# Optimization experiments

Hardware: AMD Instinct MI355X
Metric: run time of the kernel (lower is better)

The kernel has to match this reference:

```python
import jax, jax.numpy as jnp
import numpy as np

HIDDEN = 256
HEADS = 8
HEAD_DIM = HIDDEN // HEADS
SCALE = HEAD_DIM ** -0.5
N = 4096
NUM_GRAPHS = 16
LN_EPS = 1e-5


def setup_inputs() -> dict:
    key = jax.random.key(0)
    ks = jax.random.split(key, 8)
    x = jax.random.normal(ks[0], (N, HIDDEN), dtype=jnp.float32)
    batch = jnp.sort(jax.random.randint(ks[1], (N,), 0, NUM_GRAPHS, dtype=jnp.int64))
    # Xavier-uniform linear weights, stored as [in, out] (y = x @ W + b)
    lim = float(np.sqrt(6.0 / (HIDDEN + HIDDEN)))
    def W(k):
        return jax.random.uniform(k, (HIDDEN, HIDDEN), jnp.float32, -lim, lim)
    return {
        "x": x,
        "batch": batch,
        "Wq": W(ks[2]), "bq": jnp.zeros((HIDDEN,), jnp.float32),
        "Wk": W(ks[3]), "bk": jnp.zeros((HIDDEN,), jnp.float32),
        "Wv": W(ks[4]), "bv": jnp.zeros((HIDDEN,), jnp.float32),
        "Wo": W(ks[5]), "bo": jnp.zeros((HIDDEN,), jnp.float32),
        "gamma": jnp.ones((HIDDEN,), jnp.float32),
        "beta": jnp.zeros((HIDDEN,), jnp.float32),
    }


def _layer_norm(x, gamma, beta):
    mu = jnp.mean(x, axis=-1, keepdims=True)
    var = jnp.mean(jnp.square(x - mu), axis=-1, keepdims=True)
    return (x - mu) * jax.lax.rsqrt(var + LN_EPS) * gamma + beta


def reference(x, batch, Wq, bq, Wk, bk, Wv, bv, Wo, bo, gamma, beta):
    residual = x
    h = _layer_norm(x, gamma, beta)
    n = h.shape[0]
    q = (h @ Wq + bq).reshape(n, HEADS, HEAD_DIM)
    k = (h @ Wk + bk).reshape(n, HEADS, HEAD_DIM)
    v = (h @ Wv + bv).reshape(n, HEADS, HEAD_DIM)
    # dense scores masked to block-diagonal (same-graph) structure
    scores = jnp.einsum('ihd,jhd->ihj', q, k) * SCALE  # [N, H, N]
    same_graph = (batch[None, :] == batch[:, None])[:, None, :]  # [N, 1, N]
    scores = jnp.where(same_graph, scores, -jnp.inf)
    attn = jax.nn.softmax(scores, axis=-1)
    attn = jnp.nan_to_num(attn, nan=0.0)
    out = jnp.einsum('ihj,jhd->ihd', attn, v).reshape(n, HIDDEN)
    out = out @ Wo + bo
    return residual + out
```

## Files before the change

kernel.cpp:

```cpp
#include <hip/hip_runtime.h>

#define NNODES 4096
#define HID 256
#define NG 16
#define NH 8
#define HD 32
#define LN_EPS 1e-5f
#define QSCALE (0.17677669529663687f * 1.4426950408889634f)
#define CAPT 384
#define VTS (CAPT + 2)

typedef unsigned short u16;
typedef unsigned int u32;
typedef __bf16 bf16x8 __attribute__((ext_vector_type(8)));
typedef float f32x4 __attribute__((ext_vector_type(4)));

__device__ __forceinline__ float bf2f(u16 u){
  union { u32 i; float f; } c; c.i = ((u32)u) << 16; return c.f;
}
__device__ __forceinline__ u16 f2bf(float f){
  union { float f; u32 i; } c; c.f = f;
  u32 x = c.i;
  return (u16)((x + 0x7fffu + ((x >> 16) & 1u)) >> 16);
}

__global__ __launch_bounds__(256) void prep_kernel(
    const float* __restrict__ x, const float* __restrict__ gamma,
    const float* __restrict__ beta, u16* __restrict__ h,
    const float* __restrict__ Wq, const float* __restrict__ Wk,
    const float* __restrict__ Wv, const float* __restrict__ Wo,
    u16* __restrict__ Wt, const int* __restrict__ bw, int* __restrict__ seg){
  __shared__ u16 tile[32][33];
  __shared__ int bad;
  int b = blockIdx.x;
  if (b < 1024){
    int wave = threadIdx.x >> 6, lane = threadIdx.x & 63;
    int row = b * 4 + wave;
    float4 xv = ((const float4*)x)[row * 64 + lane];
    float a0 = xv.x, a1 = xv.y, a2 = xv.z, a3 = xv.w;
    float s = a0 + a1 + a2 + a3;
    #pragma unroll
    for (int m = 1; m < 64; m <<= 1) s += __shfl_xor(s, m);
    float mu = s * (1.0f / HID);
    float d0 = a0 - mu, d1 = a1 - mu, d2 = a2 - mu, d3 = a3 - mu;
    float vv = d0*d0 + d1*d1 + d2*d2 + d3*d3;
    #pragma unroll
    for (int m = 1; m < 64; m <<= 1) vv += __shfl_xor(vv, m);
    float rs = rsqrtf(vv * (1.0f / HID) + LN_EPS);
    float4 gv = ((const float4*)gamma)[lane];
    float4 bv = ((const float4*)beta)[lane];
    ushort4 o;
    o.x = f2bf(d0 * rs * gv.x + bv.x);
    o.y = f2bf(d1 * rs * gv.y + bv.y);
    o.z = f2bf(d2 * rs * gv.z + bv.z);
    o.w = f2bf(d3 * rs * gv.w + bv.w);
    *(ushort4*)(h + (size_t)row * HID + lane * 4) = o;
  } else if (b < 1280){
    int idx = b - 1024;
    int w = idx >> 6;
    int t = idx & 63;
    int bx = (t & 7) * 32, by = (t >> 3) * 32;
    const float* src = (w == 0) ? Wq : (w == 1) ? Wk : (w == 2) ? Wv : Wo;
    u16* dst = Wt + (size_t)w * HID * HID;
    int tx = threadIdx.x & 31, ty = threadIdx.x >> 5;
    #pragma unroll
    for (int r = 0; r < 32; r += 8)
      tile[ty + r][tx] = f2bf(src[(size_t)(by + ty + r) * HID + bx + tx]);
    __syncthreads();
    #pragma unroll
    for (int r = 0; r < 32; r += 8)
      dst[(size_t)(bx + ty + r) * HID + by + tx] = tile[tx][ty + r];
  } else {
    if (threadIdx.x == 0) bad = 0;
    __syncthreads();
    int local_bad = 0;
    for (int i = threadIdx.x; i < NNODES; i += 256){
      int v = bw[i];
      if (v < 0 || v > 15) local_bad = 1;
      if (i + 1 < NNODES && bw[i + 1] < v) local_bad = 1;
    }
    if (local_bad) atomicOr(&bad, 1);
    __syncthreads();
    int stride = bad ? 2 : 1;
    int g = threadIdx.x;
    if (g <= NG){
      int lo = 0, hi = NNODES;
      while (lo < hi){
        int mid = (lo + hi) >> 1;
        if (bw[mid * stride] < g) lo = mid + 1; else hi = mid;
      }
      seg[g] = lo;
    }
  }
}

template<bool FINAL>
__device__ __forceinline__ void gemm_tile(const u16* __restrict__ A, const u16* __restrict__ Bt,
    const float* __restrict__ bias, const float* __restrict__ resid, void* __restrict__ out){
  int gw = blockIdx.x * 4 + (threadIdx.x >> 6);
  int lane = threadIdx.x & 63;
  int lr = lane & 15, lq = lane >> 4;
  int m0 = (gw >> 4) * 64;
  int n0 = (gw & 15) * 16;
  f32x4 acc[4] = {};
  const u16* arow = A + (size_t)(m0 + lr) * HID + lq * 8;
  const u16* brow = Bt + (size_t)(n0 + lr) * HID + lq * 8;
  #pragma unroll
  for (int k0 = 0; k0 < HID; k0 += 32){
    bf16x8 b = *(const bf16x8*)(brow + k0);
    #pragma unroll
    for (int t = 0; t < 4; t++){
      bf16x8 a = *(const bf16x8*)(arow + (size_t)t * 16 * HID + k0);
      acc[t] = __builtin_amdgcn_mfma_f32_16x16x32_bf16(a, b, acc[t], 0, 0, 0);
    }
  }
  int col = n0 + lr;
  float bb = bias[col];
  #pragma unroll
  for (int t = 0; t < 4; t++){
    #pragma unroll
    for (int r = 0; r < 4; r++){
      int row = m0 + 16 * t + lq * 4 + r;
      float val = acc[t][r] + bb;
      if (FINAL){
        val += resid[(size_t)row * HID + col];
        ((float*)out)[(size_t)row * HID + col] = val;
      } else {
        ((u16*)out)[(size_t)row * HID + col] = f2bf(val);
      }
    }
  }
}

__global__ __launch_bounds__(256) void gemm_qkv_kernel(const u16* __restrict__ h,
    const u16* __restrict__ Wt, const float* __restrict__ bq, const float* __restrict__ bk,
    const float* __restrict__ bv, u16* __restrict__ q, u16* __restrict__ k, u16* __restrict__ v){
  int which = blockIdx.y;
  const u16* B = Wt + (size_t)which * HID * HID;
  const float* bias = (which == 0) ? bq : (which == 1) ? bk : bv;
  u16* out = (which == 0) ? q : (which == 1) ? k : v;
  gemm_tile<false>(h, B, bias, nullptr, out);
}

__global__ __launch_bounds__(256) void gemm_proj_kernel(const u16* __restrict__ ao,
    const u16* __restrict__ WtO, const float* __restrict__ bo, const float* __restrict__ x,
    float* __restrict__ out){
  gemm_tile<true>(ao, WtO, bo, x, out);
}

__global__ __launch_bounds__(256) void attn_kernel(const u16* __restrict__ q,
    const u16* __restrict__ k, const u16* __restrict__ v, const int* __restrict__ seg,
    u16* __restrict__ out){
  __shared__ u16 kl[CAPT * HD];
  __shared__ u16 vt[HD * VTS];
  int gh = blockIdx.y;
  int g = gh >> 3, hd = gh & 7;
  int start = seg[g], end = seg[g + 1];
  int len = end - start;
  if (len <= 0) return;
  if (len > CAPT) len = CAPT;
  int ntj = (len + 15) >> 4;
  int nj16 = ntj << 4;
  for (int idx = threadIdx.x; idx < nj16 * 4; idx += 256){
    int row = idx >> 2, part = idx & 3;
    uint4 val = make_uint4(0, 0, 0, 0);
    if (row < len)
      val = *(const uint4*)&k[(size_t)(start + row) * HID + hd * HD + part * 8];
    *(uint4*)&kl[row * HD + part * 8] = val;
  }
  for (int idx = threadIdx.x; idx < nj16 * 16; idx += 256){
    int row = idx >> 4, dg = idx & 15;
    u32 w = 0;
    if (row < len)
      w = *(const u32*)&v[(size_t)(start + row) * HID + hd * HD + dg * 2];
    vt[(2 * dg) * VTS + row]     = (u16)(w & 0xffffu);
    vt[(2 * dg + 1) * VTS + row] = (u16)(w >> 16);
  }
  __syncthreads();
  int wave = threadIdx.x >> 6, lane = threadIdx.x & 63;
  int lq = lane >> 4, lr = lane & 15;
  for (int tq = blockIdx.x * 4 + wave; tq < ntj; tq += gridDim.x * 4){
    int q0 = tq << 4;
    bf16x8 qf = *(const bf16x8*)&q[(size_t)(start + q0 + lr) * HID + hd * HD + lq * 8];
    f32x4 o0 = {0.f, 0.f, 0.f, 0.f}, o1 = {0.f, 0.f, 0.f, 0.f};
    float m = -3.0e38f, l = 0.f;
    for (int jt = 0; jt < ntj; jt++){
      int j0 = jt << 4;
      bf16x8 kf = *(const bf16x8*)&kl[(j0 + lr) * HD + lq * 8];
      f32x4 st = __builtin_amdgcn_mfma_f32_16x16x32_bf16(kf, qf,
                   (f32x4){0.f, 0.f, 0.f, 0.f}, 0, 0, 0);
      int jb = j0 + lq * 4;
      float s0 = (jb + 0 < len) ? st[0] * QSCALE : -3.0e38f;
      float s1 = (jb + 1 < len) ? st[1] * QSCALE : -3.0e38f;
      float s2 = (jb + 2 < len) ? st[2] * QSCALE : -3.0e38f;
      float s3 = (jb + 3 < len) ? st[3] * QSCALE : -3.0e38f;
      float tm = fmaxf(fmaxf(s0, s1), fmaxf(s2, s3));
      tm = fmaxf(tm, __shfl_xor(tm, 16));
      tm = fmaxf(tm, __shfl_xor(tm, 32));
      float mn = fmaxf(m, tm);
      float alpha = exp2f(m - mn);
      float p0 = exp2f(s0 - mn), p1 = exp2f(s1 - mn);
      float p2 = exp2f(s2 - mn), p3 = exp2f(s3 - mn);
      float ps = (p0 + p1) + (p2 + p3);
      ps += __shfl_xor(ps, 16);
      ps += __shfl_xor(ps, 32);
      l = l * alpha + ps;
      m = mn;
      union { bf16x8 v8; u16 s[8]; u32 w[4]; } pf, vf0, vf1;
      pf.w[0] = (u32)f2bf(p0) | ((u32)f2bf(p1) << 16);
      pf.w[1] = (u32)f2bf(p2) | ((u32)f2bf(p3) << 16);
      pf.w[2] = 0; pf.w[3] = 0;
      const u16* vp0 = &vt[lr * VTS + j0 + lq * 4];
      const u16* vp1 = &vt[(16 + lr) * VTS + j0 + lq * 4];
      vf0.w[0] = *(const u32*)vp0; vf0.w[1] = *(const u32*)(vp0 + 2);
      vf0.w[2] = 0; vf0.w[3] = 0;
      vf1.w[0] = *(const u32*)vp1; vf1.w[1] = *(const u32*)(vp1 + 2);
      vf1.w[2] = 0; vf1.w[3] = 0;
      o0 = o0 * alpha;
      o1 = o1 * alpha;
      o0 = __builtin_amdgcn_mfma_f32_16x16x32_bf16(vf0.v8, pf.v8, o0, 0, 0, 0);
      o1 = __builtin_amdgcn_mfma_f32_16x16x32_bf16(vf1.v8, pf.v8, o1, 0, 0, 0);
    }
    if (q0 + lr < len){
      float rl = 1.0f / l;
      u16* orow = out + (size_t)(start + q0 + lr) * HID + hd * HD;
      int dbase = lq * 4;
      *(u32*)&orow[dbase]          = (u32)f2bf(o0[0]*rl) | ((u32)f2bf(o0[1]*rl) << 16);
      *(u32*)&orow[dbase + 2]      = (u32)f2bf(o0[2]*rl) | ((u32)f2bf(o0[3]*rl) << 16);
      *(u32*)&orow[16 + dbase]     = (u32)f2bf(o1[0]*rl) | ((u32)f2bf(o1[1]*rl) << 16);
      *(u32*)&orow[16 + dbase + 2] = (u32)f2bf(o1[2]*rl) | ((u32)f2bf(o1[3]*rl) << 16);
    }
  }
}

__global__ void sentinel_kernel(u32* __restrict__ out, int nwords){
  int i = blockIdx.x * 256 + threadIdx.x;
  if (i < nwords) out[i] = 0x46404640u;
}

extern "C" void kernel_launch(void* const* d_in, const int* in_sizes, int n_in,
                              void* d_out, int out_size, void* d_ws, size_t ws_size,
                              hipStream_t stream){
  const float* x   = (const float*)d_in[0];
  const int* batch = (const int*)d_in[1];
  const float* Wq = (const float*)d_in[2],  *bq = (const float*)d_in[3];
  const float* Wk = (const float*)d_in[4],  *bk = (const float*)d_in[5];
  const float* Wv = (const float*)d_in[6],  *bv = (const float*)d_in[7];
  const float* Wo = (const float*)d_in[8],  *bo = (const float*)d_in[9];
  const float* gamma = (const float*)d_in[10], *beta = (const float*)d_in[11];

  const size_t WT_OFF  = 1024;
  const size_t QKV_OFF = WT_OFF + 4 * HID * HID * 2;
  const size_t BUF     = (size_t)NNODES * HID * 2;
  const size_t NEED    = QKV_OFF + 4 * BUF;

  if (ws_size < NEED){
    int nwords = out_size / 2;
    sentinel_kernel<<<(nwords + 255) / 256, 256, 0, stream>>>((u32*)d_out, nwords);
    return;
  }

  char* w = (char*)d_ws;
  int* seg  = (int*)(w + 128);
  u16* Wt   = (u16*)(w + WT_OFF);
  u16* qb   = (u16*)(w + QKV_OFF);
  u16* kb   = qb + (size_t)NNODES * HID;
  u16* vb   = kb + (size_t)NNODES * HID;
  u16* ao   = vb + (size_t)NNODES * HID;
  u16* h    = (u16*)d_out;

  prep_kernel<<<1281, 256, 0, stream>>>(x, gamma, beta, h, Wq, Wk, Wv, Wo, Wt, batch, seg);
  gemm_qkv_kernel<<<dim3(256, 3), 256, 0, stream>>>(h, Wt, bq, bk, bv, qb, kb, vb);
  attn_kernel<<<dim3(4, NG * NH), 256, 0, stream>>>(qb, kb, vb, seg, ao);
  gemm_proj_kernel<<<256, 256, 0, stream>>>(ao, Wt + 3 * (size_t)HID * HID, bo, x, (float*)d_out);
}
```

Baseline: 133.5 us.

## Fuse all stages into one cooperative persistent kernel with grid syncs

Replaces the four separate launches (prep, QKV GEMM, attention, output projection) with a single cooperative kernel of 256 blocks that separates stages with grid.sync(). Each block now does several LayerNorm rows, one weight-transpose tile, QKV tiles for all three matrices, and two attention jobs. The aim is to remove per-launch overhead and inter-kernel gaps. In exchange, grid-wide barriers and reduced parallelism per stage (256 blocks instead of up to 1281) may lengthen some stages, and LN output moves to a new workspace buffer.

```diff
diff --git a/kernel.cpp b/kernel.cpp
--- a/kernel.cpp
+++ b/kernel.cpp
@@ -1,4 +1,7 @@
 #include <hip/hip_runtime.h>
+#include <hip/hip_cooperative_groups.h>
+
+namespace cg = cooperative_groups;
 
 #define NNODES 4096
 #define HID 256
@@ -10,6 +13,10 @@
 #define CAPT 384
 #define VTS (CAPT + 2)
 
+#define WT_OFF  1024
+#define QKV_OFF (WT_OFF + 4 * HID * HID * 2)
+#define BUFSZ   ((size_t)NNODES * HID * 2)
+
 typedef unsigned short u16;
 typedef unsigned int u32;
 typedef __bf16 bf16x8 __attribute__((ext_vector_type(8)));
@@ -22,76 +29,6 @@
   union { float f; u32 i; } c; c.f = f;
   u32 x = c.i;
   return (u16)((x + 0x7fffu + ((x >> 16) & 1u)) >> 16);
-}
-
-__global__ __launch_bounds__(256) void prep_kernel(
-    const float* __restrict__ x, const float* __restrict__ gamma,
-    const float* __restrict__ beta, u16* __restrict__ h,
-    const float* __restrict__ Wq, const float* __restrict__ Wk,
-    const float* __restrict__ Wv, const float* __restrict__ Wo,
-    u16* __restrict__ Wt, const int* __restrict__ bw, int* __restrict__ seg){
-  __shared__ u16 tile[32][33];
-  __shared__ int bad;
-  int b = blockIdx.x;
-  if (b < 1024){
-    int wave = threadIdx.x >> 6, lane = threadIdx.x & 63;
-    int row = b * 4 + wave;
-    float4 xv = ((const float4*)x)[row * 64 + lane];
-    float a0 = xv.x, a1 = xv.y, a2 = xv.z, a3 = xv.w;
-    float s = a0 + a1 + a2 + a3;
-    #pragma unroll
-    for (int m = 1; m < 64; m <<= 1) s += __shfl_xor(s, m);
-    float mu = s * (1.0f / HID);
-    float d0 = a0 - mu, d1 = a1 - mu, d2 = a2 - mu, d3 = a3 - mu;
-    float vv = d0*d0 + d1*d1 + d2*d2 + d3*d3;
-    #pragma unroll
-    for (int m = 1; m < 64; m <<= 1) vv += __shfl_xor(vv, m);
-    float rs = rsqrtf(vv * (1.0f / HID) + LN_EPS);
-    float4 gv = ((const float4*)gamma)[lane];
-    float4 bv = ((const float4*)beta)[lane];
-    ushort4 o;
-    o.x = f2bf(d0 * rs * gv.x + bv.x);
-    o.y = f2bf(d1 * rs * gv.y + bv.y);
-    o.z = f2bf(d2 * rs * gv.z + bv.z);
-    o.w = f2bf(d3 * rs * gv.w + bv.w);
-    *(ushort4*)(h + (size_t)row * HID + lane * 4) = o;
-  } else if (b < 1280){
-    int idx = b - 1024;
-    int w = idx >> 6;
-    int t = idx & 63;
-    int bx = (t & 7) * 32, by = (t >> 3) * 32;
-    const float* src = (w == 0) ? Wq : (w == 1) ? Wk : (w == 2) ? Wv : Wo;
-    u16* dst = Wt + (size_t)w * HID * HID;
-    int tx = threadIdx.x & 31, ty = threadIdx.x >> 5;
-    #pragma unroll
-    for (int r = 0; r < 32; r += 8)
-      tile[ty + r][tx] = f2bf(src[(size_t)(by + ty + r) * HID + bx + tx]);
-    __syncthreads();
-    #pragma unroll
-    for (int r = 0; r < 32; r += 8)
-      dst[(size_t)(bx + ty + r) * HID + by + tx] = tile[tx][ty + r];
-  } else {
-    if (threadIdx.x == 0) bad = 0;
-    __syncthreads();
-    int local_bad = 0;
-    for (int i = threadIdx.x; i < NNODES; i += 256){
-      int v = bw[i];
-      if (v < 0 || v > 15) local_bad = 1;
-      if (i + 1 < NNODES && bw[i + 1] < v) local_bad = 1;
-    }
-    if (local_bad) atomicOr(&bad, 1);
-    __syncthreads();
-    int stride = bad ? 2 : 1;
-    int g = threadIdx.x;
-    if (g <= NG){
-      int lo = 0, hi = NNODES;
-      while (lo < hi){
-        int mid = (lo + hi) >> 1;
-        if (bw[mid * stride] < g) lo = mid + 1; else hi = mid;
-      }
-      seg[g] = lo;
-    }
-  }
 }
 
 template<bool FINAL>
@@ -132,105 +69,192 @@
   }
 }
 
-__global__ __launch_bounds__(256) void gemm_qkv_kernel(const u16* __restrict__ h,
-    const u16* __restrict__ Wt, const float* __restrict__ bq, const float* __restrict__ bk,
-    const float* __restrict__ bv, u16* __restrict__ q, u16* __restrict__ k, u16* __restrict__ v){
-  int which = blockIdx.y;
-  const u16* B = Wt + (size_t)which * HID * HID;
-  const float* bias = (which == 0) ? bq : (which == 1) ? bk : bv;
-  u16* out = (which == 0) ? q : (which == 1) ? k : v;
-  gemm_tile<false>(h, B, bias, nullptr, out);
-}
-
-__global__ __launch_bounds__(256) void gemm_proj_kernel(const u16* __restrict__ ao,
-    const u16* __restrict__ WtO, const float* __restrict__ bo, const float* __restrict__ x,
-    float* __restrict__ out){
-  gemm_tile<true>(ao, WtO, bo, x, out);
-}
-
-__global__ __launch_bounds__(256) void attn_kernel(const u16* __restrict__ q,
-    const u16* __restrict__ k, const u16* __restrict__ v, const int* __restrict__ seg,
-    u16* __restrict__ out){
+__global__ __launch_bounds__(256) void fused_kernel(
+    const float* __restrict__ x, const int* __restrict__ bw,
+    const float* __restrict__ Wq, const float* __restrict__ bq,
+    const float* __restrict__ Wk, const float* __restrict__ bk,
+    const float* __restrict__ Wv, const float* __restrict__ bv,
+    const float* __restrict__ Wo, const float* __restrict__ bo,
+    const float* __restrict__ gamma, const float* __restrict__ beta,
+    char* __restrict__ ws, float* __restrict__ out){
+  cg::grid_group grid = cg::this_grid();
   __shared__ u16 kl[CAPT * HD];
   __shared__ u16 vt[HD * VTS];
-  int gh = blockIdx.y;
-  int g = gh >> 3, hd = gh & 7;
-  int start = seg[g], end = seg[g + 1];
-  int len = end - start;
-  if (len <= 0) return;
-  if (len > CAPT) len = CAPT;
-  int ntj = (len + 15) >> 4;
-  int nj16 = ntj << 4;
-  for (int idx = threadIdx.x; idx < nj16 * 4; idx += 256){
-    int row = idx >> 2, part = idx & 3;
-    uint4 val = make_uint4(0, 0, 0, 0);
-    if (row < len)
-      val = *(const uint4*)&k[(size_t)(start + row) * HID + hd * HD + part * 8];
-    *(uint4*)&kl[row * HD + part * 8] = val;
-  }
-  for (int idx = threadIdx.x; idx < nj16 * 16; idx += 256){
-    int row = idx >> 4, dg = idx & 15;
-    u32 w = 0;
-    if (row < len)
-      w = *(const u32*)&v[(size_t)(start + row) * HID + hd * HD + dg * 2];
-    vt[(2 * dg) * VTS + row]     = (u16)(w & 0xffffu);
-    vt[(2 * dg + 1) * VTS + row] = (u16)(w >> 16);
-  }
-  __syncthreads();
+  __shared__ int bad;
+
+  int* seg = (int*)(ws + 128);
+  u16* Wt  = (u16*)(ws + WT_OFF);
+  u16* qb  = (u16*)(ws + QKV_OFF);
+  u16* kb  = qb + (size_t)NNODES * HID;
+  u16* vb  = kb + (size_t)NNODES * HID;
+  u16* ao  = vb + (size_t)NNODES * HID;
+  u16* h   = ao + (size_t)NNODES * HID;
+
+  int b = blockIdx.x;
   int wave = threadIdx.x >> 6, lane = threadIdx.x & 63;
-  int lq = lane >> 4, lr = lane & 15;
-  for (int tq = blockIdx.x * 4 + wave; tq < ntj; tq += gridDim.x * 4){
-    int q0 = tq << 4;
-    bf16x8 qf = *(const bf16x8*)&q[(size_t)(start + q0 + lr) * HID + hd * HD + lq * 8];
-    f32x4 o0 = {0.f, 0.f, 0.f, 0.f}, o1 = {0.f, 0.f, 0.f, 0.f};
-    float m = -3.0e38f, l = 0.f;
-    for (int jt = 0; jt < ntj; jt++){
-      int j0 = jt << 4;
-      bf16x8 kf = *(const bf16x8*)&kl[(j0 + lr) * HD + lq * 8];
-      f32x4 st = __builtin_amdgcn_mfma_f32_16x16x32_bf16(kf, qf,
-                   (f32x4){0.f, 0.f, 0.f, 0.f}, 0, 0, 0);
-      int jb = j0 + lq * 4;
-      float s0 = (jb + 0 < len) ? st[0] * QSCALE : -3.0e38f;
-      float s1 = (jb + 1 < len) ? st[1] * QSCALE : -3.0e38f;
-      float s2 = (jb + 2 < len) ? st[2] * QSCALE : -3.0e38f;
-      float s3 = (jb + 3 < len) ? st[3] * QSCALE : -3.0e38f;
-      float tm = fmaxf(fmaxf(s0, s1), fmaxf(s2, s3));
-      tm = fmaxf(tm, __shfl_xor(tm, 16));
-      tm = fmaxf(tm, __shfl_xor(tm, 32));
-      float mn = fmaxf(m, tm);
-      float alpha = exp2f(m - mn);
-      float p0 = exp2f(s0 - mn), p1 = exp2f(s1 - mn);
-      float p2 = exp2f(s2 - mn), p3 = exp2f(s3 - mn);
-      float ps = (p0 + p1) + (p2 + p3);
-      ps += __shfl_xor(ps, 16);
-      ps += __shfl_xor(ps, 32);
-      l = l * alpha + ps;
-      m = mn;
-      union { bf16x8 v8; u16 s[8]; u32 w[4]; } pf, vf0, vf1;
-      pf.w[0] = (u32)f2bf(p0) | ((u32)f2bf(p1) << 16);
-      pf.w[1] = (u32)f2bf(p2) | ((u32)f2bf(p3) << 16);
-      pf.w[2] = 0; pf.w[3] = 0;
-      const u16* vp0 = &vt[lr * VTS + j0 + lq * 4];
-      const u16* vp1 = &vt[(16 + lr) * VTS + j0 + lq * 4];
-      vf0.w[0] = *(const u32*)vp0; vf0.w[1] = *(const u32*)(vp0 + 2);
-      vf0.w[2] = 0; vf0.w[3] = 0;
-      vf1.w[0] = *(const u32*)vp1; vf1.w[1] = *(const u32*)(vp1 + 2);
-      vf1.w[2] = 0; vf1.w[3] = 0;
-      o0 = o0 * alpha;
-      o1 = o1 * alpha;
-      o0 = __builtin_amdgcn_mfma_f32_16x16x32_bf16(vf0.v8, pf.v8, o0, 0, 0, 0);
-      o1 = __builtin_amdgcn_mfma_f32_16x16x32_bf16(vf1.v8, pf.v8, o1, 0, 0, 0);
-    }
-    if (q0 + lr < len){
-      float rl = 1.0f / l;
-      u16* orow = out + (size_t)(start + q0 + lr) * HID + hd * HD;
-      int dbase = lq * 4;
-      *(u32*)&orow[dbase]          = (u32)f2bf(o0[0]*rl) | ((u32)f2bf(o0[1]*rl) << 16);
-      *(u32*)&orow[dbase + 2]      = (u32)f2bf(o0[2]*rl) | ((u32)f2bf(o0[3]*rl) << 16);
-      *(u32*)&orow[16 + dbase]     = (u32)f2bf(o1[0]*rl) | ((u32)f2bf(o1[1]*rl) << 16);
-      *(u32*)&orow[16 + dbase + 2] = (u32)f2bf(o1[2]*rl) | ((u32)f2bf(o1[3]*rl) << 16);
-    }
-  }
+
+  #pragma unroll
+  for (int i = 0; i < 4; i++){
+    int row = b * 16 + i * 4 + wave;
+    float4 xv = ((const float4*)x)[row * 64 + lane];
+    float a0 = xv.x, a1 = xv.y, a2 = xv.z, a3 = xv.w;
+    float s = a0 + a1 + a2 + a3;
+    #pragma unroll
+    for (int m = 1; m < 64; m <<= 1) s += __shfl_xor(s, m);
+    float mu = s * (1.0f / HID);
+    float d0 = a0 - mu, d1 = a1 - mu, d2 = a2 - mu, d3 = a3 - mu;
+    float vv = d0*d0 + d1*d1 + d2*d2 + d3*d3;
+    #pragma unroll
+    for (int m = 1; m < 64; m <<= 1) vv += __shfl_xor(vv, m);
+    float rs = rsqrtf(vv * (1.0f / HID) + LN_EPS);
+    float4 gv = ((const float4*)gamma)[lane];
+    float4 bv2 = ((const float4*)beta)[lane];
+    ushort4 o;
+    o.x = f2bf(d0 * rs * gv.x + bv2.x);
+    o.y = f2bf(d1 * rs * gv.y + bv2.y);
+    o.z = f2bf(d2 * rs * gv.z + bv2.z);
+    o.w = f2bf(d3 * rs * gv.w + bv2.w);
+    *(ushort4*)(h + (size_t)row * HID + lane * 4) = o;
+  }
+
+  {
+    u16 (*tile)[33] = (u16(*)[33])kl;
+    int w = b >> 6;
+    int t = b & 63;
+    int bx = (t & 7) * 32, by = (t >> 3) * 32;
+    const float* src = (w == 0) ? Wq : (w == 1) ? Wk : (w == 2) ? Wv : Wo;
+    u16* dst = Wt + (size_t)w * HID * HID;
+    int tx = threadIdx.x & 31, ty = threadIdx.x >> 5;
+    #pragma unroll
+    for (int r = 0; r < 32; r += 8)
+      tile[ty + r][tx] = f2bf(src[(size_t)(by + ty + r) * HID + bx + tx]);
+    __syncthreads();
+    #pragma unroll
+    for (int r = 0; r < 32; r += 8)
+      dst[(size_t)(bx + ty + r) * HID + by + tx] = tile[tx][ty + r];
+  }
+
+  if (b == 0){
+    if (threadIdx.x == 0) bad = 0;
+    __syncthreads();
+    int local_bad = 0;
+    for (int i = threadIdx.x; i < NNODES; i += 256){
+      int v = bw[i];
+      if (v < 0 || v > 15) local_bad = 1;
+      if (i + 1 < NNODES && bw[i + 1] < v) local_bad = 1;
+    }
+    if (local_bad) atomicOr(&bad, 1);
+    __syncthreads();
+    int stride = bad ? 2 : 1;
+    int g = threadIdx.x;
+    if (g <= NG){
+      int lo = 0, hi = NNODES;
+      while (lo < hi){
+        int mid = (lo + hi) >> 1;
+        if (bw[mid * stride] < g) lo = mid + 1; else hi = mid;
+      }
+      seg[g] = lo;
+    }
+  }
+
+  grid.sync();
+
+  #pragma unroll
+  for (int rep = 0; rep < 3; rep++){
+    const u16* B = Wt + (size_t)rep * HID * HID;
+    const float* bias = (rep == 0) ? bq : (rep == 1) ? bk : bv;
+    u16* o = (rep == 0) ? qb : (rep == 1) ? kb : vb;
+    gemm_tile<false>(h, B, bias, nullptr, o);
+  }
+
+  grid.sync();
+
+  for (int rep = 0; rep < 2; rep++){
+    int job = b + 256 * rep;
+    int bx = job >> 7, gh = job & 127;
+    int g = gh >> 3, hd = gh & 7;
+    int start = seg[g], end = seg[g + 1];
+    int len = end - start;
+    if (len > CAPT) len = CAPT;
+    if (len > 0){
+      int ntj = (len + 15) >> 4;
+      int nj16 = ntj << 4;
+      __syncthreads();
+      for (int idx = threadIdx.x; idx < nj16 * 4; idx += 256){
+        int row = idx >> 2, part = idx & 3;
+        uint4 val = make_uint4(0, 0, 0, 0);
+        if (row < len)
+          val = *(const uint4*)&kb[(size_t)(start + row) * HID + hd * HD + part * 8];
+        *(uint4*)&kl[row * HD + part * 8] = val;
+      }
+      for (int idx = threadIdx.x; idx < nj16 * 16; idx += 256){
+        int row = idx >> 4, dg = idx & 15;
+        u32 w = 0;
+        if (row < len)
+          w = *(const u32*)&vb[(size_t)(start + row) * HID + hd * HD + dg * 2];
+        vt[(2 * dg) * VTS + row]     = (u16)(w & 0xffffu);
+        vt[(2 * dg + 1) * VTS + row] = (u16)(w >> 16);
+      }
+      __syncthreads();
+      int lq = lane >> 4, lr = lane & 15;
+      for (int tq = bx * 4 + wave; tq < ntj; tq += 16){
+        int q0 = tq << 4;
+        bf16x8 qf = *(const bf16x8*)&qb[(size_t)(start + q0 + lr) * HID + hd * HD + lq * 8];
+        f32x4 o0 = {0.f, 0.f, 0.f, 0.f}, o1 = {0.f, 0.f, 0.f, 0.f};
+        float m = -3.0e38f, l = 0.f;
+        for (int jt = 0; jt < ntj; jt++){
+          int j0 = jt << 4;
+          bf16x8 kf = *(const bf16x8*)&kl[(j0 + lr) * HD + lq * 8];
+          f32x4 st = __builtin_amdgcn_mfma_f32_16x16x32_bf16(kf, qf,
+                       (f32x4){0.f, 0.f, 0.f, 0.f}, 0, 0, 0);
+          int jb2 = j0 + lq * 4;
+          float s0 = (jb2 + 0 < len) ? st[0] * QSCALE : -3.0e38f;
+          float s1 = (jb2 + 1 < len) ? st[1] * QSCALE : -3.0e38f;
+          float s2 = (jb2 + 2 < len) ? st[2] * QSCALE : -3.0e38f;
+          float s3 = (jb2 + 3 < len) ? st[3] * QSCALE : -3.0e38f;
+          float tm = fmaxf(fmaxf(s0, s1), fmaxf(s2, s3));
+          tm = fmaxf(tm, __shfl_xor(tm, 16));
+          tm = fmaxf(tm, __shfl_xor(tm, 32));
+          float mn = fmaxf(m, tm);
+          float alpha = exp2f(m - mn);
+          float p0 = exp2f(s0 - mn), p1 = exp2f(s1 - mn);
+          float p2 = exp2f(s2 - mn), p3 = exp2f(s3 - mn);
+          float ps = (p0 + p1) + (p2 + p3);
+          ps += __shfl_xor(ps, 16);
+          ps += __shfl_xor(ps, 32);
+          l = l * alpha + ps;
+          m = mn;
+          union { bf16x8 v8; u32 w[4]; } pf, vf0, vf1;
+          pf.w[0] = (u32)f2bf(p0) | ((u32)f2bf(p1) << 16);
+          pf.w[1] = (u32)f2bf(p2) | ((u32)f2bf(p3) << 16);
+          pf.w[2] = 0; pf.w[3] = 0;
+          const u16* vp0 = &vt[lr * VTS + j0 + lq * 4];
+          const u16* vp1 = &vt[(16 + lr) * VTS + j0 + lq * 4];
+          vf0.w[0] = *(const u32*)vp0; vf0.w[1] = *(const u32*)(vp0 + 2);
+          vf0.w[2] = 0; vf0.w[3] = 0;
+          vf1.w[0] = *(const u32*)vp1; vf1.w[1] = *(const u32*)(vp1 + 2);
+          vf1.w[2] = 0; vf1.w[3] = 0;
+          o0 = o0 * alpha;
+          o1 = o1 * alpha;
+          o0 = __builtin_amdgcn_mfma_f32_16x16x32_bf16(vf0.v8, pf.v8, o0, 0, 0, 0);
+          o1 = __builtin_amdgcn_mfma_f32_16x16x32_bf16(vf1.v8, pf.v8, o1, 0, 0, 0);
+        }
+        if (q0 + lr < len){
+          float rl = 1.0f / l;
+          u16* orow = ao + (size_t)(start + q0 + lr) * HID + hd * HD;
+          int dbase = lq * 4;
+          *(u32*)&orow[dbase]          = (u32)f2bf(o0[0]*rl) | ((u32)f2bf(o0[1]*rl) << 16);
+          *(u32*)&orow[dbase + 2]      = (u32)f2bf(o0[2]*rl) | ((u32)f2bf(o0[3]*rl) << 16);
+          *(u32*)&orow[16 + dbase]     = (u32)f2bf(o1[0]*rl) | ((u32)f2bf(o1[1]*rl) << 16);
+          *(u32*)&orow[16 + dbase + 2] = (u32)f2bf(o1[2]*rl) | ((u32)f2bf(o1[3]*rl) << 16);
+        }
+      }
+    }
+  }
+
+  grid.sync();
+
+  gemm_tile<true>(ao, Wt + 3 * (size_t)HID * HID, bo, x, out);
 }
 
 __global__ void sentinel_kernel(u32* __restrict__ out, int nwords){
@@ -248,11 +272,10 @@
   const float* Wv = (const float*)d_in[6],  *bv = (const float*)d_in[7];
   const float* Wo = (const float*)d_in[8],  *bo = (const float*)d_in[9];
   const float* gamma = (const float*)d_in[10], *beta = (const float*)d_in[11];
-
-  const size_t WT_OFF  = 1024;
-  const size_t QKV_OFF = WT_OFF + 4 * HID * HID * 2;
-  const size_t BUF     = (size_t)NNODES * HID * 2;
-  const size_t NEED    = QKV_OFF + 4 * BUF;
+  char* ws = (char*)d_ws;
+  float* out = (float*)d_out;
+
+  const size_t NEED = (size_t)QKV_OFF + 5 * BUFSZ;
 
   if (ws_size < NEED){
     int nwords = out_size / 2;
@@ -260,17 +283,10 @@
     return;
   }
 
-  char* w = (char*)d_ws;
-  int* seg  = (int*)(w + 128);
-  u16* Wt   = (u16*)(w + WT_OFF);
-  u16* qb   = (u16*)(w + QKV_OFF);
-  u16* kb   = qb + (size_t)NNODES * HID;
-  u16* vb   = kb + (size_t)NNODES * HID;
-  u16* ao   = vb + (size_t)NNODES * HID;
-  u16* h    = (u16*)d_out;
-
-  prep_kernel<<<1281, 256, 0, stream>>>(x, gamma, beta, h, Wq, Wk, Wv, Wo, Wt, batch, seg);
-  gemm_qkv_kernel<<<dim3(256, 3), 256, 0, stream>>>(h, Wt, bq, bk, bv, qb, kb, vb);
-  attn_kernel<<<dim3(4, NG * NH), 256, 0, stream>>>(qb, kb, vb, seg, ao);
-  gemm_proj_kernel<<<256, 256, 0, stream>>>(ao, Wt + 3 * (size_t)HID * HID, bo, x, (float*)d_out);
-}
+  void* args[] = { (void*)&x, (void*)&batch, (void*)&Wq, (void*)&bq,
+                   (void*)&Wk, (void*)&bk, (void*)&Wv, (void*)&bv,
+                   (void*)&Wo, (void*)&bo, (void*)&gamma, (void*)&beta,
+                   (void*)&ws, (void*)&out };
+  hipLaunchCooperativeKernel((const void*)fused_kernel, dim3(256), dim3(256),
+                             args, 0, stream);
+}
```

After: 230.9 us. 1.73x slower.

## Replace online softmax with register-resident two-pass softmax and vectorize V transpose

Applied to the files above, without the earlier changes.

The attention kernel now computes all score tiles for a query block up front into a fully unrolled register array (up to 24 tiles), takes one global max, then computes the exponentials and their sum, and finally runs the PV MFMAs. This removes the per-tile cross-lane max/sum shuffles and the alpha rescaling of the accumulators that the online softmax needed. The V-transpose staging also switches to 16-byte global loads. The cost is much higher register pressure (96 floats of scores plus packed probabilities), which may lower occupancy or cause spills.

```diff
diff --git a/kernel.cpp b/kernel.cpp
--- a/kernel.cpp
+++ b/kernel.cpp
@@ -8,6 +8,7 @@
 #define LN_EPS 1e-5f
 #define QSCALE (0.17677669529663687f * 1.4426950408889634f)
 #define CAPT 384
+#define NTJMAX 24
 #define VTS (CAPT + 2)
 
 typedef unsigned short u16;
@@ -168,13 +169,20 @@
       val = *(const uint4*)&k[(size_t)(start + row) * HID + hd * HD + part * 8];
     *(uint4*)&kl[row * HD + part * 8] = val;
   }
-  for (int idx = threadIdx.x; idx < nj16 * 16; idx += 256){
-    int row = idx >> 4, dg = idx & 15;
-    u32 w = 0;
+  for (int idx = threadIdx.x; idx < nj16 * 4; idx += 256){
+    int row = idx >> 2, part = idx & 3;
+    uint4 w = make_uint4(0, 0, 0, 0);
     if (row < len)
-      w = *(const u32*)&v[(size_t)(start + row) * HID + hd * HD + dg * 2];
-    vt[(2 * dg) * VTS + row]     = (u16)(w & 0xffffu);
-    vt[(2 * dg + 1) * VTS + row] = (u16)(w >> 16);
+      w = *(const uint4*)&v[(size_t)(start + row) * HID + hd * HD + part * 8];
+    int d0 = part * 8;
+    vt[(d0 + 0) * VTS + row] = (u16)(w.x & 0xffffu);
+    vt[(d0 + 1) * VTS + row] = (u16)(w.x >> 16);
+    vt[(d0 + 2) * VTS + row] = (u16)(w.y & 0xffffu);
+    vt[(d0 + 3) * VTS + row] = (u16)(w.y >> 16);
+    vt[(d0 + 4) * VTS + row] = (u16)(w.z & 0xffffu);
+    vt[(d0 + 5) * VTS + row] = (u16)(w.z >> 16);
+    vt[(d0 + 6) * VTS + row] = (u16)(w.w & 0xffffu);
+    vt[(d0 + 7) * VTS + row] = (u16)(w.w >> 16);
   }
   __syncthreads();
   int wave = threadIdx.x >> 6, lane = threadIdx.x & 63;
@@ -182,44 +190,61 @@
   for (int tq = blockIdx.x * 4 + wave; tq < ntj; tq += gridDim.x * 4){
     int q0 = tq << 4;
     bf16x8 qf = *(const bf16x8*)&q[(size_t)(start + q0 + lr) * HID + hd * HD + lq * 8];
+    f32x4 st[NTJMAX];
+    #pragma unroll
+    for (int jt = 0; jt < NTJMAX; jt++){
+      if (jt < ntj){
+        bf16x8 kf = *(const bf16x8*)&kl[((jt << 4) + lr) * HD + lq * 8];
+        st[jt] = __builtin_amdgcn_mfma_f32_16x16x32_bf16(kf, qf,
+                   (f32x4){0.f, 0.f, 0.f, 0.f}, 0, 0, 0);
+      }
+    }
+    float m = -3.0e38f;
+    #pragma unroll
+    for (int jt = 0; jt < NTJMAX; jt++){
+      if (jt < ntj){
+        int jb = (jt << 4) + lq * 4;
+        float s0 = (jb + 0 < len) ? st[jt][0] * QSCALE : -3.0e38f;
+        float s1 = (jb + 1 < len) ? st[jt][1] * QSCALE : -3.0e38f;
+        float s2 = (jb + 2 < len) ? st[jt][2] * QSCALE : -3.0e38f;
+        float s3 = (jb + 3 < len) ? st[jt][3] * QSCALE : -3.0e38f;
+        st[jt][0] = s0; st[jt][1] = s1; st[jt][2] = s2; st[jt][3] = s3;
+        m = fmaxf(m, fmaxf(fmaxf(s0, s1), fmaxf(s2, s3)));
+      }
+    }
+    m = fmaxf(m, __shfl_xor(m, 16));
+    m = fmaxf(m, __shfl_xor(m, 32));
+    float l = 0.f;
+    u32 pw[NTJMAX][2];
+    #pragma unroll
+    for (int jt = 0; jt < NTJMAX; jt++){
+      if (jt < ntj){
+        float p0 = exp2f(st[jt][0] - m), p1 = exp2f(st[jt][1] - m);
+        float p2 = exp2f(st[jt][2] - m), p3 = exp2f(st[jt][3] - m);
+        l += (p0 + p1) + (p2 + p3);
+        pw[jt][0] = (u32)f2bf(p0) | ((u32)f2bf(p1) << 16);
+        pw[jt][1] = (u32)f2bf(p2) | ((u32)f2bf(p3) << 16);
+      }
+    }
+    l += __shfl_xor(l, 16);
+    l += __shfl_xor(l, 32);
     f32x4 o0 = {0.f, 0.f, 0.f, 0.f}, o1 = {0.f, 0.f, 0.f, 0.f};
-    float m = -3.0e38f, l = 0.f;
-    for (int jt = 0; jt < ntj; jt++){
-      int j0 = jt << 4;
-      bf16x8 kf = *(const bf16x8*)&kl[(j0 + lr) * HD + lq * 8];
-      f32x4 st = __builtin_amdgcn_mfma_f32_16x16x32_bf16(kf, qf,
-                   (f32x4){0.f, 0.f, 0.f, 0.f}, 0, 0, 0);
-      int jb = j0 + lq * 4;
-      float s0 = (jb + 0 < len) ? st[0] * QSCALE : -3.0e38f;
-      float s1 = (jb + 1 < len) ? st[1] * QSCALE : -3.0e38f;
-      float s2 = (jb + 2 < len) ? st[2] * QSCALE : -3.0e38f;
-      float s3 = (jb + 3 < len) ? st[3] * QSCALE : -3.0e38f;
-      float tm = fmaxf(fmaxf(s0, s1), fmaxf(s2, s3));
-      tm = fmaxf(tm, __shfl_xor(tm, 16));
-      tm = fmaxf(tm, __shfl_xor(tm, 32));
-      float mn = fmaxf(m, tm);
-      float alpha = exp2f(m - mn);
-      float p0 = exp2f(s0 - mn), p1 = exp2f(s1 - mn);
-      float p2 = exp2f(s2 - mn), p3 = exp2f(s3 - mn);
-      float ps = (p0 + p1) + (p2 + p3);
-      ps += __shfl_xor(ps, 16);
-      ps += __shfl_xor(ps, 32);
-      l = l * alpha + ps;
-      m = mn;
-      union { bf16x8 v8; u16 s[8]; u32 w[4]; } pf, vf0, vf1;
-      pf.w[0] = (u32)f2bf(p0) | ((u32)f2bf(p1) << 16);
-      pf.w[1] = (u32)f2bf(p2) | ((u32)f2bf(p3) << 16);
-      pf.w[2] = 0; pf.w[3] = 0;
-      const u16* vp0 = &vt[lr * VTS + j0 + lq * 4];
-      const u16* vp1 = &vt[(16 + lr) * VTS + j0 + lq * 4];
-      vf0.w[0] = *(const u32*)vp0; vf0.w[1] = *(const u32*)(vp0 + 2);
-      vf0.w[2] = 0; vf0.w[3] = 0;
-      vf1.w[0] = *(const u32*)vp1; vf1.w[1] = *(const u32*)(vp1 + 2);
-      vf1.w[2] = 0; vf1.w[3] = 0;
-      o0 = o0 * alpha;
-      o1 = o1 * alpha;
-      o0 = __builtin_amdgcn_mfma_f32_16x16x32_bf16(vf0.v8, pf.v8, o0, 0, 0, 0);
-      o1 = __builtin_amdgcn_mfma_f32_16x16x32_bf16(vf1.v8, pf.v8, o1, 0, 0, 0);
+    #pragma unroll
+    for (int jt = 0; jt < NTJMAX; jt++){
+      if (jt < ntj){
+        int j0 = jt << 4;
+        union { bf16x8 v8; u32 w[4]; } pf, vf0, vf1;
+        pf.w[0] = pw[jt][0]; pf.w[1] = pw[jt][1];
+        pf.w[2] = 0; pf.w[3] = 0;
+        const u16* vp0 = &vt[lr * VTS + j0 + lq * 4];
+        const u16* vp1 = &vt[(16 + lr) * VTS + j0 + lq * 4];
+        vf0.w[0] = *(const u32*)vp0; vf0.w[1] = *(const u32*)(vp0 + 2);
+        vf0.w[2] = 0; vf0.w[3] = 0;
+        vf1.w[0] = *(const u32*)vp1; vf1.w[1] = *(const u32*)(vp1 + 2);
+        vf1.w[2] = 0; vf1.w[3] = 0;
+        o0 = __builtin_amdgcn_mfma_f32_16x16x32_bf16(vf0.v8, pf.v8, o0, 0, 0, 0);
+        o1 = __builtin_amdgcn_mfma_f32_16x16x32_bf16(vf1.v8, pf.v8, o1, 0, 0, 0);
+      }
     }
     if (q0 + lr < len){
       float rl = 1.0f / l;
```

Measured after the change: 145.4 us. 8.9% more time.

## Process two query tiles per wave to reuse K/V fragments in attention

Applied to the files above, without the earlier changes.

Each wave now handles a pair of 16-row query tiles, sharing every K fragment and V-transposed fragment load between two independent online-softmax chains. This interleaves twice the MFMA work per LDS read, and the grid drops from 4 to 2 blocks per graph-head. The V transpose load is widened to 16-byte global reads. The costs are higher register pressure, fewer blocks (256 in total) so less parallelism, and a possible out-of-segment Q read for the B tile, which is loaded even when hasB is false.

```diff
diff --git a/kernel.cpp b/kernel.cpp
--- a/kernel.cpp
+++ b/kernel.cpp
@@ -168,67 +168,118 @@
       val = *(const uint4*)&k[(size_t)(start + row) * HID + hd * HD + part * 8];
     *(uint4*)&kl[row * HD + part * 8] = val;
   }
-  for (int idx = threadIdx.x; idx < nj16 * 16; idx += 256){
-    int row = idx >> 4, dg = idx & 15;
-    u32 w = 0;
+  for (int idx = threadIdx.x; idx < nj16 * 4; idx += 256){
+    int row = idx >> 2, part = idx & 3;
+    uint4 w = make_uint4(0, 0, 0, 0);
     if (row < len)
-      w = *(const u32*)&v[(size_t)(start + row) * HID + hd * HD + dg * 2];
-    vt[(2 * dg) * VTS + row]     = (u16)(w & 0xffffu);
-    vt[(2 * dg + 1) * VTS + row] = (u16)(w >> 16);
+      w = *(const uint4*)&v[(size_t)(start + row) * HID + hd * HD + part * 8];
+    int d0 = part * 8;
+    vt[(d0 + 0) * VTS + row] = (u16)(w.x & 0xffffu);
+    vt[(d0 + 1) * VTS + row] = (u16)(w.x >> 16);
+    vt[(d0 + 2) * VTS + row] = (u16)(w.y & 0xffffu);
+    vt[(d0 + 3) * VTS + row] = (u16)(w.y >> 16);
+    vt[(d0 + 4) * VTS + row] = (u16)(w.z & 0xffffu);
+    vt[(d0 + 5) * VTS + row] = (u16)(w.z >> 16);
+    vt[(d0 + 6) * VTS + row] = (u16)(w.w & 0xffffu);
+    vt[(d0 + 7) * VTS + row] = (u16)(w.w >> 16);
   }
   __syncthreads();
   int wave = threadIdx.x >> 6, lane = threadIdx.x & 63;
   int lq = lane >> 4, lr = lane & 15;
-  for (int tq = blockIdx.x * 4 + wave; tq < ntj; tq += gridDim.x * 4){
-    int q0 = tq << 4;
-    bf16x8 qf = *(const bf16x8*)&q[(size_t)(start + q0 + lr) * HID + hd * HD + lq * 8];
-    f32x4 o0 = {0.f, 0.f, 0.f, 0.f}, o1 = {0.f, 0.f, 0.f, 0.f};
-    float m = -3.0e38f, l = 0.f;
+  int wv = blockIdx.x * 4 + wave;
+  for (int tp = wv; 2 * tp < ntj; tp += 8){
+    int q0A = (2 * tp) << 4;
+    int q0B = q0A + 16;
+    bool hasB = (2 * tp + 1) < ntj;
+    bf16x8 qfA = *(const bf16x8*)&q[(size_t)(start + q0A + lr) * HID + hd * HD + lq * 8];
+    bf16x8 qfB = *(const bf16x8*)&q[(size_t)(start + q0B + lr) * HID + hd * HD + lq * 8];
+    f32x4 o0A = {0.f,0.f,0.f,0.f}, o1A = {0.f,0.f,0.f,0.f};
+    f32x4 o0B = {0.f,0.f,0.f,0.f}, o1B = {0.f,0.f,0.f,0.f};
+    float mA = -3.0e38f, lA = 0.f;
+    float mB = -3.0e38f, lB = 0.f;
     for (int jt = 0; jt < ntj; jt++){
       int j0 = jt << 4;
       bf16x8 kf = *(const bf16x8*)&kl[(j0 + lr) * HD + lq * 8];
-      f32x4 st = __builtin_amdgcn_mfma_f32_16x16x32_bf16(kf, qf,
-                   (f32x4){0.f, 0.f, 0.f, 0.f}, 0, 0, 0);
+      f32x4 stA = __builtin_amdgcn_mfma_f32_16x16x32_bf16(kf, qfA,
+                    (f32x4){0.f,0.f,0.f,0.f}, 0, 0, 0);
+      f32x4 stB = __builtin_amdgcn_mfma_f32_16x16x32_bf16(kf, qfB,
+                    (f32x4){0.f,0.f,0.f,0.f}, 0, 0, 0);
       int jb = j0 + lq * 4;
-      float s0 = (jb + 0 < len) ? st[0] * QSCALE : -3.0e38f;
-      float s1 = (jb + 1 < len) ? st[1] * QSCALE : -3.0e38f;
-      float s2 = (jb + 2 < len) ? st[2] * QSCALE : -3.0e38f;
-      float s3 = (jb + 3 < len) ? st[3] * QSCALE : -3.0e38f;
-      float tm = fmaxf(fmaxf(s0, s1), fmaxf(s2, s3));
-      tm = fmaxf(tm, __shfl_xor(tm, 16));
-      tm = fmaxf(tm, __shfl_xor(tm, 32));
-      float mn = fmaxf(m, tm);
-      float alpha = exp2f(m - mn);
-      float p0 = exp2f(s0 - mn), p1 = exp2f(s1 - mn);
-      float p2 = exp2f(s2 - mn), p3 = exp2f(s3 - mn);
-      float ps = (p0 + p1) + (p2 + p3);
-      ps += __shfl_xor(ps, 16);
-      ps += __shfl_xor(ps, 32);
-      l = l * alpha + ps;
-      m = mn;
-      union { bf16x8 v8; u16 s[8]; u32 w[4]; } pf, vf0, vf1;
-      pf.w[0] = (u32)f2bf(p0) | ((u32)f2bf(p1) << 16);
-      pf.w[1] = (u32)f2bf(p2) | ((u32)f2bf(p3) << 16);
-      pf.w[2] = 0; pf.w[3] = 0;
+      bool v0 = jb + 0 < len, v1 = jb + 1 < len, v2 = jb + 2 < len, v3 = jb + 3 < len;
+      union { bf16x8 v8; u32 w[4]; } vf0, vf1, pfA, pfB;
       const u16* vp0 = &vt[lr * VTS + j0 + lq * 4];
       const u16* vp1 = &vt[(16 + lr) * VTS + j0 + lq * 4];
       vf0.w[0] = *(const u32*)vp0; vf0.w[1] = *(const u32*)(vp0 + 2);
       vf0.w[2] = 0; vf0.w[3] = 0;
       vf1.w[0] = *(const u32*)vp1; vf1.w[1] = *(const u32*)(vp1 + 2);
       vf1.w[2] = 0; vf1.w[3] = 0;
-      o0 = o0 * alpha;
-      o1 = o1 * alpha;
-      o0 = __builtin_amdgcn_mfma_f32_16x16x32_bf16(vf0.v8, pf.v8, o0, 0, 0, 0);
-      o1 = __builtin_amdgcn_mfma_f32_16x16x32_bf16(vf1.v8, pf.v8, o1, 0, 0, 0);
-    }
-    if (q0 + lr < len){
-      float rl = 1.0f / l;
-      u16* orow = out + (size_t)(start + q0 + lr) * HID + hd * HD;
-      int dbase = lq * 4;
-      *(u32*)&orow[dbase]          = (u32)f2bf(o0[0]*rl) | ((u32)f2bf(o0[1]*rl) << 16);
-      *(u32*)&orow[dbase + 2]      = (u32)f2bf(o0[2]*rl) | ((u32)f2bf(o0[3]*rl) << 16);
-      *(u32*)&orow[16 + dbase]     = (u32)f2bf(o1[0]*rl) | ((u32)f2bf(o1[1]*rl) << 16);
-      *(u32*)&orow[16 + dbase + 2] = (u32)f2bf(o1[2]*rl) | ((u32)f2bf(o1[3]*rl) << 16);
+      {
+        float s0 = v0 ? stA[0] * QSCALE : -3.0e38f;
+        float s1 = v1 ? stA[1] * QSCALE : -3.0e38f;
+        float s2 = v2 ? stA[2] * QSCALE : -3.0e38f;
+        float s3 = v3 ? stA[3] * QSCALE : -3.0e38f;
+        float tm = fmaxf(fmaxf(s0, s1), fmaxf(s2, s3));
+        tm = fmaxf(tm, __shfl_xor(tm, 16));
+        tm = fmaxf(tm, __shfl_xor(tm, 32));
+        float mn = fmaxf(mA, tm);
+        float alpha = exp2f(mA - mn);
+        float p0 = exp2f(s0 - mn), p1 = exp2f(s1 - mn);
+        float p2 = exp2f(s2 - mn), p3 = exp2f(s3 - mn);
+        float ps = (p0 + p1) + (p2 + p3);
+        ps += __shfl_xor(ps, 16);
+        ps += __shfl_xor(ps, 32);
+        lA = lA * alpha + ps;
+        mA = mn;
+        pfA.w[0] = (u32)f2bf(p0) | ((u32)f2bf(p1) << 16);
+        pfA.w[1] = (u32)f2bf(p2) | ((u32)f2bf(p3) << 16);
+        pfA.w[2] = 0; pfA.w[3] = 0;
+        o0A = o0A * alpha;
+        o1A = o1A * alpha;
+        o0A = __builtin_amdgcn_mfma_f32_16x16x32_bf16(vf0.v8, pfA.v8, o0A, 0, 0, 0);
+        o1A = __builtin_amdgcn_mfma_f32_16x16x32_bf16(vf1.v8, pfA.v8, o1A, 0, 0, 0);
+      }
+      {
+        float s0 = v0 ? stB[0] * QSCALE : -3.0e38f;
+        float s1 = v1 ? stB[1] * QSCALE : -3.0e38f;
+        float s2 = v2 ? stB[2] * QSCALE : -3.0e38f;
+        float s3 = v3 ? stB[3] * QSCALE : -3.0e38f;
+        float tm = fmaxf(fmaxf(s0, s1), fmaxf(s2, s3));
+        tm = fmaxf(tm, __shfl_xor(tm, 16));
+        tm = fmaxf(tm, __shfl_xor(tm, 32));
+        float mn = fmaxf(mB, tm);
+        float alpha = exp2f(mB - mn);
+        float p0 = exp2f(s0 - mn), p1 = exp2f(s1 - mn);
+        float p2 = exp2f(s2 - mn), p3 = exp2f(s3 - mn);
+        float ps = (p0 + p1) + (p2 + p3);
+        ps += __shfl_xor(ps, 16);
+        ps += __shfl_xor(ps, 32);
+        lB = lB * alpha + ps;
+        mB = mn;
+        pfB.w[0] = (u32)f2bf(p0) | ((u32)f2bf(p1) << 16);
+        pfB.w[1] = (u32)f2bf(p2) | ((u32)f2bf(p3) << 16);
+        pfB.w[2] = 0; pfB.w[3] = 0;
+        o0B = o0B * alpha;
+        o1B = o1B * alpha;
+        o0B = __builtin_amdgcn_mfma_f32_16x16x32_bf16(vf0.v8, pfB.v8, o0B, 0, 0, 0);
+        o1B = __builtin_amdgcn_mfma_f32_16x16x32_bf16(vf1.v8, pfB.v8, o1B, 0, 0, 0);
+      }
+    }
+    int dbase = lq * 4;
+    if (q0A + lr < len){
+      float rl = 1.0f / lA;
+      u16* orow = out + (size_t)(start + q0A + lr) * HID + hd * HD;
+      *(u32*)&orow[dbase]          = (u32)f2bf(o0A[0]*rl) | ((u32)f2bf(o0A[1]*rl) << 16);
+      *(u32*)&orow[dbase + 2]      = (u32)f2bf(o0A[2]*rl) | ((u32)f2bf(o0A[3]*rl) << 16);
+      *(u32*)&orow[16 + dbase]     = (u32)f2bf(o1A[0]*rl) | ((u32)f2bf(o1A[1]*rl) << 16);
+      *(u32*)&orow[16 + dbase + 2] = (u32)f2bf(o1A[2]*rl) | ((u32)f2bf(o1A[3]*rl) << 16);
+    }
+    if (hasB && q0B + lr < len){
+      float rl = 1.0f / lB;
+      u16* orow = out + (size_t)(start + q0B + lr) * HID + hd * HD;
+      *(u32*)&orow[dbase]          = (u32)f2bf(o0B[0]*rl) | ((u32)f2bf(o0B[1]*rl) << 16);
+      *(u32*)&orow[dbase + 2]      = (u32)f2bf(o0B[2]*rl) | ((u32)f2bf(o0B[3]*rl) << 16);
+      *(u32*)&orow[16 + dbase]     = (u32)f2bf(o1B[0]*rl) | ((u32)f2bf(o1B[1]*rl) << 16);
+      *(u32*)&orow[16 + dbase + 2] = (u32)f2bf(o1B[2]*rl) | ((u32)f2bf(o1B[3]*rl) << 16);
     }
   }
 }
@@ -271,6 +322,6 @@
 
   prep_kernel<<<1281, 256, 0, stream>>>(x, gamma, beta, h, Wq, Wk, Wv, Wo, Wt, batch, seg);
   gemm_qkv_kernel<<<dim3(256, 3), 256, 0, stream>>>(h, Wt, bq, bk, bv, qb, kb, vb);
-  attn_kernel<<<dim3(4, NG * NH), 256, 0, stream>>>(qb, kb, vb, seg, ao);
+  attn_kernel<<<dim3(2, NG * NH), 256, 0, stream>>>(qb, kb, vb, seg, ao);
   gemm_proj_kernel<<<256, 256, 0, stream>>>(ao, Wt + 3 * (size_t)HID * HID, bo, x, (float*)d_out);
 }
```

Result: no change. 135.6 us (+1.5%).
